# Optimization experiments

Hardware: AMD Instinct MI355X
Metric: run time of the kernel (lower is better)

Reference implementation:

```python
import jax, jax.numpy as jnp
import numpy as np

N_NODES = 100000
N_EDGES = 1600000
NFEAT, NHID, NCLASS = 256, 128, 40


def setup_inputs() -> dict:
    key = jax.random.key(0)
    ks = jax.random.split(key, 8)
    x = jax.random.normal(ks[0], (N_NODES, NFEAT), dtype=jnp.float32)
    edge_src = jax.random.randint(ks[1], (N_EDGES,), 0, N_NODES, dtype=jnp.int32)
    edge_dst = jax.random.randint(ks[2], (N_EDGES,), 0, N_NODES, dtype=jnp.int32)
    edge_weight = jax.random.uniform(ks[3], (N_EDGES,), dtype=jnp.float32)
    W1 = jax.random.normal(ks[4], (NFEAT, NHID), dtype=jnp.float32) * (1.0 / np.sqrt(NFEAT))
    b1 = jnp.zeros((NHID,), dtype=jnp.float32)
    W2 = jax.random.normal(ks[5], (NHID, NCLASS), dtype=jnp.float32) * (1.0 / np.sqrt(NHID))
    b2 = jnp.zeros((NCLASS,), dtype=jnp.float32)
    return {"x": x, "edge_src": edge_src, "edge_dst": edge_dst,
            "edge_weight": edge_weight, "W1": W1, "b1": b1, "W2": W2, "b2": b2}


def _spmm(edge_src, edge_dst, edge_weight, h):
    # out[i] = sum_{e: dst[e]==i} w[e] * h[src[e]]  (sparse adj @ h)
    msgs = edge_weight[:, None] * h[edge_src]            # [E, D]
    return jax.ops.segment_sum(msgs, edge_dst, num_segments=N_NODES)


def reference(x, edge_src, edge_dst, edge_weight, W1, b1, W2, b2):
    # GraphConvolution 1: adj @ (x @ W1) + b1, then ReLU
    h = _spmm(edge_src, edge_dst, edge_weight, x @ W1) + b1
    h = jax.nn.relu(h)
    # Dropout(p=0.5) is identity in eval/deterministic reference
    # GraphConvolution 2: adj @ (h @ W2) + b2
    out = _spmm(edge_src, edge_dst, edge_weight, h @ W2) + b2
    return out
```

## Files before the change

### kernel.cpp

```cpp
#include <hip/hip_runtime.h>

#define N_NODES 100000
#define N_EDGES 1600000
#define NFEAT 256
#define NHID 128
#define NCLASS 40

#define NGROUP 8
#define NODES_PER_GROUP 12500
#define NBKT 128
#define NPB 782
#define KPB (NPB * 8)
#define BCAP2 13200
#define EPB2 8192
#define NCH2 ((N_EDGES + EPB2 - 1) / EPB2)
#define NGEMM1 ((N_NODES + 127) / 128)
#define NKEY (N_NODES * 8)

using short8 = __attribute__((ext_vector_type(8))) short;
using f32x4 = __attribute__((ext_vector_type(4))) float;
using i32x4 = __attribute__((ext_vector_type(4))) int;
using i32x2 = __attribute__((ext_vector_type(2))) int;

__device__ inline float blo(unsigned u) { return __uint_as_float(u << 16); }
__device__ inline float bhi(unsigned u) { return __uint_as_float(u & 0xffff0000u); }
__device__ inline unsigned pk2(float a, float b) {
  unsigned x = __float_as_uint(a), y = __float_as_uint(b);
  unsigned lo = (x + 0x7FFFu + ((x >> 16) & 1u)) >> 16;
  unsigned hi = (y + 0x7FFFu + ((y >> 16) & 1u)) >> 16;
  return lo | (hi << 16);
}
__device__ inline unsigned short pk1(float a) {
  unsigned x = __float_as_uint(a);
  return (unsigned short)((x + 0x7FFFu + ((x >> 16) & 1u)) >> 16);
}


__global__ __launch_bounds__(512) void k_fatA(const int* __restrict__ src,
                                              const int* __restrict__ dst,
                                              const float* __restrict__ w,
                                              int* __restrict__ bcnt,
                                              int* __restrict__ bktK,
                                              i32x2* __restrict__ bktSW,
                                              const float* __restrict__ W1,
                                              unsigned short* __restrict__ w1s) {
  int tid = threadIdx.x;
  if (blockIdx.x >= NCH2) {
    int t = (blockIdx.x - NCH2) * 512 + tid;
    if (t < NFEAT * NHID) {
      int k = t >> 7, c = t & 127;
      int idx = (c * 256 + k) ^ ((c & 7) << 3);
      w1s[idx] = pk1(W1[t]);
    }
    return;
  }
  __shared__ int lcnt[NBKT], loff[NBKT], lcur[NBKT], lbase[NBKT];
  __shared__ int eK[EPB2];
  __shared__ i32x2 eSW[EPB2];
  if (tid < NBKT) lcnt[tid] = 0;
  __syncthreads();

  int base_e = blockIdx.x * EPB2;
  int nE = N_EDGES - base_e;
  if (nE > EPB2) nE = EPB2;
  int e0 = base_e + tid * 16;
  int key[16];
  i32x2 sw[16];
  bool full = (tid * 16 + 16 <= nE);
  if (full) {
#pragma unroll
    for (int g = 0; g < 4; g++) {
      i32x4 d4 = __builtin_nontemporal_load((const i32x4*)(dst + e0 + g * 4));
      i32x4 s4 = __builtin_nontemporal_load((const i32x4*)(src + e0 + g * 4));
      f32x4 w4 = __builtin_nontemporal_load((const f32x4*)(w + e0 + g * 4));
      int dd[4] = {d4.x, d4.y, d4.z, d4.w};
      int ss[4] = {s4.x, s4.y, s4.z, s4.w};
      float ww[4] = {w4.x, w4.y, w4.z, w4.w};
#pragma unroll
      for (int i = 0; i < 4; i++) {
        key[g * 4 + i] = dd[i] * 8 + (int)((unsigned)ss[i] / NODES_PER_GROUP);
        sw[g * 4 + i].x = ss[i];
        sw[g * 4 + i].y = __float_as_int(ww[i]);
        atomicAdd(&lcnt[(unsigned)dd[i] / NPB], 1);
      }
    }
  } else {
#pragma unroll
    for (int i = 0; i < 16; i++) {
      int e = tid * 16 + i;
      if (e < nE) {
        int d = dst[base_e + e], s = src[base_e + e];
        float ww = w[base_e + e];
        key[i] = d * 8 + (int)((unsigned)s / NODES_PER_GROUP);
        sw[i].x = s;
        sw[i].y = __float_as_int(ww);
        atomicAdd(&lcnt[(unsigned)d / NPB], 1);
      } else {
        key[i] = -1;
      }
    }
  }
  __syncthreads();
  if (tid < NBKT) loff[tid] = lcnt[tid];
  __syncthreads();
  for (int off = 1; off < NBKT; off <<= 1) {
    int u = (tid < NBKT && tid >= off) ? loff[tid - off] : 0;
    __syncthreads();
    if (tid < NBKT) loff[tid] += u;
    __syncthreads();
  }
  if (tid < NBKT) {
    int excl = loff[tid] - lcnt[tid];
    loff[tid] = excl;
    lcur[tid] = excl;
    lbase[tid] = atomicAdd(&bcnt[tid], lcnt[tid]);
  }
  __syncthreads();
#pragma unroll
  for (int i = 0; i < 16; i++) {
    if (key[i] >= 0) {
      int b = (unsigned)key[i] / KPB;
      int p = atomicAdd(&lcur[b], 1);
      eK[p] = key[i];
      eSW[p] = sw[i];
    }
  }
  __syncthreads();
  int wid = tid >> 6, lane = tid & 63;
  for (int b = wid; b < NBKT; b += 8) {
    int cnt = lcnt[b];
    int l0 = loff[b];
    int gb = lbase[b];
    if (gb + cnt > BCAP2) cnt = BCAP2 - gb;
    size_t g0 = (size_t)b * BCAP2 + gb;
    for (int i = lane; i < cnt; i += 64) {
      bktK[g0 + i] = eK[l0 + i];
      bktSW[g0 + i] = eSW[l0 + i];
    }
  }
}


__global__ __launch_bounds__(256) void k_gemm1(const float* __restrict__ x,
                                               const uint4* __restrict__ w1s,
                                               unsigned* __restrict__ h1u) {
  __shared__ char sB[65536];
  int tid = threadIdx.x;
  {
    uint4* dd = (uint4*)sB;
    for (int i = 0; i < 16; i++) dd[tid + i * 256] = w1s[tid + i * 256];
  }
  __syncthreads();

  int lane = tid & 63, wid = tid >> 6;
  int r16 = lane & 15, kgrp = lane >> 4;
  int rowbase = blockIdx.x * 128 + wid * 32;
  int ra0 = min(rowbase + r16, N_NODES - 1);
  int ra1 = min(rowbase + 16 + r16, N_NODES - 1);

  f32x4 acc[2][8];
#pragma unroll
  for (int m = 0; m < 2; m++)
#pragma unroll
    for (int n = 0; n < 8; n++) acc[m][n] = (f32x4){0.f, 0.f, 0.f, 0.f};

  for (int kt8 = 0; kt8 < 8; kt8++) {
    int k0 = kt8 * 32 + kgrp * 8;
    union { uint4 u; short8 s; } a[2];
#pragma unroll
    for (int m = 0; m < 2; m++) {
      const float* ap = x + (size_t)(m ? ra1 : ra0) * NFEAT + k0;
      float4 v0 = *(const float4*)ap;
      float4 v1 = *(const float4*)(ap + 4);
      a[m].u.x = pk2(v0.x, v0.y);
      a[m].u.y = pk2(v0.z, v0.w);
      a[m].u.z = pk2(v1.x, v1.y);
      a[m].u.w = pk2(v1.z, v1.w);
    }
#pragma unroll
    for (int n = 0; n < 8; n++) {
      int c = 16 * n + r16;
      int off = (c * 512 + k0 * 2) ^ ((c & 7) << 4);
      short8 b = *(const short8*)(sB + off);
      acc[0][n] = __builtin_amdgcn_mfma_f32_16x16x32_bf16(a[0].s, b, acc[0][n], 0, 0, 0);
      acc[1][n] = __builtin_amdgcn_mfma_f32_16x16x32_bf16(a[1].s, b, acc[1][n], 0, 0, 0);
    }
  }

#pragma unroll
  for (int m = 0; m < 2; m++) {
    int rb = rowbase + m * 16 + kgrp * 4;
#pragma unroll
    for (int n = 0; n < 8; n++) {
      f32x4 v = acc[m][n];
#pragma unroll
      for (int j = 0; j < 4; j++) {
        float o = __shfl_xor(v[j], 1);
        int row = rb + j;
        if (!(lane & 1) && row < N_NODES)
          h1u[(size_t)row * 64 + 8 * n + (r16 >> 1)] = pk2(v[j], o);
      }
    }
  }
}


__global__ void k_bbase(const int* __restrict__ bcnt, int* __restrict__ bbase) {
  __shared__ int s[NBKT];
  int t = threadIdx.x;
  int v = bcnt[t];
  s[t] = v;
  __syncthreads();
  for (int off = 1; off < NBKT; off <<= 1) {
    int u = (t >= off) ? s[t - off] : 0;
    __syncthreads();
    s[t] += u;
    __syncthreads();
  }
  bbase[t] = s[t] - v;
}


__global__ __launch_bounds__(1024) void k_build(const int* __restrict__ bcnt,
                                                const int* __restrict__ bbase,
                                                const int* __restrict__ bktK,
                                                const i32x2* __restrict__ bktSW,
                                                int* __restrict__ rp2,
                                                i32x2* __restrict__ esw) {
  __shared__ int lh[KPB];
  __shared__ int partial[1024];
  __shared__ i32x2 ebuf[BCAP2];

  int b = blockIdx.x;
  int t = threadIdx.x;
  int cnt = min(bcnt[b], BCAP2);
  int base = bbase[b];
  const int* kb = bktK + (size_t)b * BCAP2;
  const i32x2* sb = bktSW + (size_t)b * BCAP2;
  int k0 = b * KPB;

  for (int i = t; i < KPB; i += 1024) lh[i] = 0;
  __syncthreads();
  for (int i = t; i < cnt; i += 1024) atomicAdd(&lh[kb[i] - k0], 1);
  __syncthreads();

  int myoff = t * 7;
  int vals[7];
  int s0 = 0;
#pragma unroll
  for (int q = 0; q < 7; q++) {
    int i = myoff + q;
    int v = (i < KPB) ? lh[i] : 0;
    vals[q] = s0;
    s0 += v;
  }
  partial[t] = s0;
  __syncthreads();
  for (int off = 1; off < 1024; off <<= 1) {
    int u = (t >= off) ? partial[t - off] : 0;
    __syncthreads();
    partial[t] += u;
    __syncthreads();
  }
  int excl_base = partial[t] - s0;
  __syncthreads();
#pragma unroll
  for (int q = 0; q < 7; q++) {
    int i = myoff + q;
    if (i < KPB) {
      int e = excl_base + vals[q];
      int gk = k0 + i;
      if (gk < NKEY) rp2[gk] = base + e;
    }
  }
  __syncthreads();
#pragma unroll
  for (int q = 0; q < 7; q++) {
    int i = myoff + q;
    if (i < KPB) lh[i] = excl_base + vals[q];
  }
  if (b == NBKT - 1 && t == 0) rp2[NKEY] = N_EDGES;
  __syncthreads();

  for (int i = t; i < cnt; i += 1024) {
    int lk = kb[i] - k0;
    int pos = atomicAdd(&lh[lk], 1);
    ebuf[pos] = sb[i];
  }
  __syncthreads();

  i32x2* dstp = esw + base;
  for (int i = t; i < cnt; i += 1024) dstp[i] = ebuf[i];
}


__global__ __launch_bounds__(256) void k_spmm1(const unsigned* __restrict__ h1u,
                                               const int* __restrict__ rp2,
                                               const i32x2* __restrict__ esw,
                                               const float* __restrict__ bias1,
                                               unsigned* __restrict__ houtu) {
  int node = (blockIdx.x * 256 + threadIdx.x) >> 6;
  int lane = threadIdx.x & 63;
  if (node >= N_NODES) return;
  int beg = rp2[node * 8], end = rp2[node * 8 + 8];
  float aL0 = 0.f, aL1 = 0.f, aL2 = 0.f, aL3 = 0.f;
  float aH0 = 0.f, aH1 = 0.f, aH2 = 0.f, aH3 = 0.f;
  int j = beg;
  for (; j + 7 < end; j += 8) {
    i32x2 e0 = esw[j],     e1 = esw[j + 1], e2 = esw[j + 2], e3 = esw[j + 3];
    i32x2 e4 = esw[j + 4], e5 = esw[j + 5], e6 = esw[j + 6], e7 = esw[j + 7];
    unsigned u0 = h1u[((unsigned)e0.x << 6) + lane];
    unsigned u1 = h1u[((unsigned)e1.x << 6) + lane];
    unsigned u2 = h1u[((unsigned)e2.x << 6) + lane];
    unsigned u3 = h1u[((unsigned)e3.x << 6) + lane];
    unsigned u4 = h1u[((unsigned)e4.x << 6) + lane];
    unsigned u5 = h1u[((unsigned)e5.x << 6) + lane];
    unsigned u6 = h1u[((unsigned)e6.x << 6) + lane];
    unsigned u7 = h1u[((unsigned)e7.x << 6) + lane];
    float w0 = __int_as_float(e0.y), w1 = __int_as_float(e1.y);
    float w2 = __int_as_float(e2.y), w3 = __int_as_float(e3.y);
    float w4 = __int_as_float(e4.y), w5 = __int_as_float(e5.y);
    float w6 = __int_as_float(e6.y), w7 = __int_as_float(e7.y);
    aL0 = fmaf(w0, blo(u0), aL0); aH0 = fmaf(w0, bhi(u0), aH0);
    aL1 = fmaf(w1, blo(u1), aL1); aH1 = fmaf(w1, bhi(u1), aH1);
    aL2 = fmaf(w2, blo(u2), aL2); aH2 = fmaf(w2, bhi(u2), aH2);
    aL3 = fmaf(w3, blo(u3), aL3); aH3 = fmaf(w3, bhi(u3), aH3);
    aL0 = fmaf(w4, blo(u4), aL0); aH0 = fmaf(w4, bhi(u4), aH0);
    aL1 = fmaf(w5, blo(u5), aL1); aH1 = fmaf(w5, bhi(u5), aH1);
    aL2 = fmaf(w6, blo(u6), aL2); aH2 = fmaf(w6, bhi(u6), aH2);
    aL3 = fmaf(w7, blo(u7), aL3); aH3 = fmaf(w7, bhi(u7), aH3);
  }
  for (; j + 3 < end; j += 4) {
    i32x2 e0 = esw[j], e1 = esw[j + 1], e2 = esw[j + 2], e3 = esw[j + 3];
    unsigned u0 = h1u[((unsigned)e0.x << 6) + lane];
    unsigned u1 = h1u[((unsigned)e1.x << 6) + lane];
    unsigned u2 = h1u[((unsigned)e2.x << 6) + lane];
    unsigned u3 = h1u[((unsigned)e3.x << 6) + lane];
    float w0 = __int_as_float(e0.y), w1 = __int_as_float(e1.y);
    float w2 = __int_as_float(e2.y), w3 = __int_as_float(e3.y);
    aL0 = fmaf(w0, blo(u0), aL0); aH0 = fmaf(w0, bhi(u0), aH0);
    aL1 = fmaf(w1, blo(u1), aL1); aH1 = fmaf(w1, bhi(u1), aH1);
    aL2 = fmaf(w2, blo(u2), aL2); aH2 = fmaf(w2, bhi(u2), aH2);
    aL3 = fmaf(w3, blo(u3), aL3); aH3 = fmaf(w3, bhi(u3), aH3);
  }
  for (; j < end; j++) {
    i32x2 e0 = esw[j];
    unsigned u0 = h1u[((unsigned)e0.x << 6) + lane];
    float w0 = __int_as_float(e0.y);
    aL0 = fmaf(w0, blo(u0), aL0); aH0 = fmaf(w0, bhi(u0), aH0);
  }
  float r0 = (aL0 + aL1) + (aL2 + aL3) + bias1[2 * lane];
  float r1 = (aH0 + aH1) + (aH2 + aH3) + bias1[2 * lane + 1];
  houtu[(size_t)node * 64 + lane] = pk2(fmaxf(r0, 0.f), fmaxf(r1, 0.f));
}


__global__ __launch_bounds__(256) void k_gemm2(const unsigned* __restrict__ h_u,
                                               const float* __restrict__ W2,
                                               unsigned short* __restrict__ h2b) {
  __shared__ float hs[32][132];
  __shared__ float w2t[40][132];
  int tid = threadIdx.x;
  int row0 = blockIdx.x * 32;
  for (int i = tid; i < NHID * NCLASS; i += 256) {
    int k = i / NCLASS, c = i % NCLASS;
    w2t[c][k] = W2[i];
  }
  for (int i = tid; i < 2048; i += 256) {
    int r = i >> 6, c = i & 63;
    unsigned u = h_u[(size_t)(row0 + r) * 64 + c];
    hs[r][2 * c] = blo(u);
    hs[r][2 * c + 1] = bhi(u);
  }
  __syncthreads();
  int r = tid >> 3;
  int c0 = (tid & 7) * 5;
  float acc[5] = {0, 0, 0, 0, 0};
  for (int k = 0; k < NHID; k += 4) {
    float4 a = *(float4*)&hs[r][k];
#pragma unroll
    for (int j = 0; j < 5; j++) {
      float4 b = *(float4*)&w2t[c0 + j][k];
      acc[j] += a.x * b.x + a.y * b.y + a.z * b.z + a.w * b.w;
    }
  }
#pragma unroll
  for (int j = 0; j < 5; j++) h2b[(size_t)(row0 + r) * NCLASS + c0 + j] = pk1(acc[j]);
}


__global__ __launch_bounds__(256) void k_spmm2(const unsigned* __restrict__ h2u,
                                               const int* __restrict__ rp2,
                                               const i32x2* __restrict__ esw,
                                               const float* __restrict__ b2,
                                               float* __restrict__ out) {
  int node = (blockIdx.x * 256 + threadIdx.x) >> 6;
  int lane = threadIdx.x & 63;
  if (node >= N_NODES) return;
  int beg = rp2[node * 8], end = rp2[node * 8 + 8];
  int g = lane / 20;
  int jj = lane - g * 20;
  float aA0 = 0.f, aB0 = 0.f, aA1 = 0.f, aB1 = 0.f;
  if (g < 3) {
    int e = beg + g;
    for (; e + 3 < end; e += 6) {
      i32x2 p0 = esw[e];
      i32x2 p1 = esw[e + 3];
      unsigned u0 = h2u[(size_t)p0.x * 20 + jj];
      unsigned u1 = h2u[(size_t)p1.x * 20 + jj];
      float w0 = __int_as_float(p0.y), w1 = __int_as_float(p1.y);
      aA0 = fmaf(w0, blo(u0), aA0); aB0 = fmaf(w0, bhi(u0), aB0);
      aA1 = fmaf(w1, blo(u1), aA1); aB1 = fmaf(w1, bhi(u1), aB1);
    }
    if (e < end) {
      i32x2 p0 = esw[e];
      unsigned u0 = h2u[(size_t)p0.x * 20 + jj];
      float w0 = __int_as_float(p0.y);
      aA0 = fmaf(w0, blo(u0), aA0); aB0 = fmaf(w0, bhi(u0), aB0);
    }
  }
  float accA = aA0 + aA1, accB = aB0 + aB1;
  float tA = accA + __shfl(accA, lane + 20) + __shfl(accA, lane + 40);
  float tB = accB + __shfl(accB, lane + 20) + __shfl(accB, lane + 40);
  if (lane < 20) {
    float2 o = make_float2(tA + b2[2 * lane], tB + b2[2 * lane + 1]);
    *(float2*)&out[(size_t)node * NCLASS + 2 * lane] = o;
  }
}

extern "C" void kernel_launch(void* const* d_in, const int* in_sizes, int n_in,
                              void* d_out, int out_size, void* d_ws, size_t ws_size,
                              hipStream_t stream) {
  const float* x = (const float*)d_in[0];
  const int* src_in = (const int*)d_in[1];
  const int* dst_in = (const int*)d_in[2];
  const float* w_in = (const float*)d_in[3];
  const float* W1 = (const float*)d_in[4];
  const float* b1 = (const float*)d_in[5];
  const float* W2 = (const float*)d_in[6];
  const float* b2 = (const float*)d_in[7];
  float* out = (float*)d_out;

  unsigned short* h1b = (unsigned short*)d_ws;
  unsigned* hbuf = (unsigned*)(h1b + (size_t)N_NODES * NHID);
  unsigned short* h2b = (unsigned short*)(hbuf + (size_t)N_NODES * 64);
  i32x2* esw = (i32x2*)(h2b + (size_t)N_NODES * NCLASS);
  i32x2* bktSW = esw + N_EDGES;
  int* bktK = (int*)(bktSW + (size_t)NBKT * BCAP2);
  int* bcnt = bktK + (size_t)NBKT * BCAP2;
  int* bbase = bcnt + NBKT;
  int* rp2 = bbase + NBKT;
  unsigned short* w1s = (unsigned short*)(rp2 + NKEY + 4);

  hipMemsetAsync(bcnt, 0, NBKT * sizeof(int), stream);
  k_fatA<<<NCH2 + 64, 512, 0, stream>>>(src_in, dst_in, w_in, bcnt, bktK, bktSW, W1, w1s);
  k_gemm1<<<NGEMM1, 256, 0, stream>>>(x, (const uint4*)w1s, (unsigned*)h1b);
  k_bbase<<<1, NBKT, 0, stream>>>(bcnt, bbase);
  k_build<<<NBKT, 1024, 0, stream>>>(bcnt, bbase, bktK, bktSW, rp2, esw);

  k_spmm1<<<(N_NODES + 3) / 4, 256, 0, stream>>>((const unsigned*)h1b, rp2, esw, b1, hbuf);
  k_gemm2<<<N_NODES / 32, 256, 0, stream>>>(hbuf, W2, h2b);
  k_spmm2<<<(N_NODES + 3) / 4, 256, 0, stream>>>((const unsigned*)h2b, rp2, esw, b2, out);
}
```

Before: 227.8 us.

## Fold bucket scan into build, use nontemporal streams, vectorize edge loads

Removes the separate single-block prefix-scan launch by having every k_build block redundantly scan the 128 bucket counts in shared memory. Adds nontemporal load/store hints on streaming activation reads and writes in gemm1, spmm1, gemm2 and spmm2 so they are less likely to displace cached data. In spmm1, aligns the edge index to even and reads pairs of (src, weight) entries as 16-byte vectors instead of 8-byte loads. The trade-off is redundant scan work in each build block and the risk that nontemporal hints evict data that later kernels reuse.

```diff
diff --git a/kernel.cpp b/kernel.cpp
--- a/kernel.cpp
+++ b/kernel.cpp
@@ -19,6 +19,7 @@
 
 using short8 = __attribute__((ext_vector_type(8))) short;
 using f32x4 = __attribute__((ext_vector_type(4))) float;
+using f32x2 = __attribute__((ext_vector_type(2))) float;
 using i32x4 = __attribute__((ext_vector_type(4))) int;
 using i32x2 = __attribute__((ext_vector_type(2))) int;
 
@@ -170,8 +171,8 @@
 #pragma unroll
     for (int m = 0; m < 2; m++) {
       const float* ap = x + (size_t)(m ? ra1 : ra0) * NFEAT + k0;
-      float4 v0 = *(const float4*)ap;
-      float4 v1 = *(const float4*)(ap + 4);
+      f32x4 v0 = __builtin_nontemporal_load((const f32x4*)ap);
+      f32x4 v1 = __builtin_nontemporal_load((const f32x4*)(ap + 4));
       a[m].u.x = pk2(v0.x, v0.y);
       a[m].u.y = pk2(v0.z, v0.w);
       a[m].u.z = pk2(v1.x, v1.y);
@@ -198,43 +199,36 @@
         float o = __shfl_xor(v[j], 1);
         int row = rb + j;
         if (!(lane & 1) && row < N_NODES)
-          h1u[(size_t)row * 64 + 8 * n + (r16 >> 1)] = pk2(v[j], o);
+          __builtin_nontemporal_store(pk2(v[j], o),
+                                      &h1u[(size_t)row * 64 + 8 * n + (r16 >> 1)]);
       }
     }
   }
 }
 
 
-__global__ void k_bbase(const int* __restrict__ bcnt, int* __restrict__ bbase) {
-  __shared__ int s[NBKT];
-  int t = threadIdx.x;
-  int v = bcnt[t];
-  s[t] = v;
-  __syncthreads();
-  for (int off = 1; off < NBKT; off <<= 1) {
-    int u = (t >= off) ? s[t - off] : 0;
-    __syncthreads();
-    s[t] += u;
-    __syncthreads();
-  }
-  bbase[t] = s[t] - v;
-}
-
-
 __global__ __launch_bounds__(1024) void k_build(const int* __restrict__ bcnt,
-                                                const int* __restrict__ bbase,
                                                 const int* __restrict__ bktK,
                                                 const i32x2* __restrict__ bktSW,
                                                 int* __restrict__ rp2,
                                                 i32x2* __restrict__ esw) {
   __shared__ int lh[KPB];
   __shared__ int partial[1024];
+  __shared__ int sc[NBKT];
   __shared__ i32x2 ebuf[BCAP2];
 
   int b = blockIdx.x;
   int t = threadIdx.x;
+  if (t < NBKT) sc[t] = bcnt[t];
+  __syncthreads();
+  for (int off = 1; off < NBKT; off <<= 1) {
+    int u = (t < NBKT && t >= off) ? sc[t - off] : 0;
+    __syncthreads();
+    if (t < NBKT) sc[t] += u;
+    __syncthreads();
+  }
+  int base = (b == 0) ? 0 : sc[b - 1];
   int cnt = min(bcnt[b], BCAP2);
-  int base = bbase[b];
   const int* kb = bktK + (size_t)b * BCAP2;
   const i32x2* sb = bktSW + (size_t)b * BCAP2;
   int k0 = b * KPB;
@@ -306,21 +300,30 @@
   float aL0 = 0.f, aL1 = 0.f, aL2 = 0.f, aL3 = 0.f;
   float aH0 = 0.f, aH1 = 0.f, aH2 = 0.f, aH3 = 0.f;
   int j = beg;
+  if ((j & 1) && j < end) {
+    i32x2 e0 = esw[j];
+    unsigned u0 = h1u[((unsigned)e0.x << 6) + lane];
+    float w0 = __int_as_float(e0.y);
+    aL0 = fmaf(w0, blo(u0), aL0); aH0 = fmaf(w0, bhi(u0), aH0);
+    j++;
+  }
   for (; j + 7 < end; j += 8) {
-    i32x2 e0 = esw[j],     e1 = esw[j + 1], e2 = esw[j + 2], e3 = esw[j + 3];
-    i32x2 e4 = esw[j + 4], e5 = esw[j + 5], e6 = esw[j + 6], e7 = esw[j + 7];
-    unsigned u0 = h1u[((unsigned)e0.x << 6) + lane];
-    unsigned u1 = h1u[((unsigned)e1.x << 6) + lane];
-    unsigned u2 = h1u[((unsigned)e2.x << 6) + lane];
-    unsigned u3 = h1u[((unsigned)e3.x << 6) + lane];
-    unsigned u4 = h1u[((unsigned)e4.x << 6) + lane];
-    unsigned u5 = h1u[((unsigned)e5.x << 6) + lane];
-    unsigned u6 = h1u[((unsigned)e6.x << 6) + lane];
-    unsigned u7 = h1u[((unsigned)e7.x << 6) + lane];
-    float w0 = __int_as_float(e0.y), w1 = __int_as_float(e1.y);
-    float w2 = __int_as_float(e2.y), w3 = __int_as_float(e3.y);
-    float w4 = __int_as_float(e4.y), w5 = __int_as_float(e5.y);
-    float w6 = __int_as_float(e6.y), w7 = __int_as_float(e7.y);
+    i32x4 q0 = *(const i32x4*)(esw + j);
+    i32x4 q1 = *(const i32x4*)(esw + j + 2);
+    i32x4 q2 = *(const i32x4*)(esw + j + 4);
+    i32x4 q3 = *(const i32x4*)(esw + j + 6);
+    unsigned u0 = h1u[((unsigned)q0.x << 6) + lane];
+    unsigned u1 = h1u[((unsigned)q0.z << 6) + lane];
+    unsigned u2 = h1u[((unsigned)q1.x << 6) + lane];
+    unsigned u3 = h1u[((unsigned)q1.z << 6) + lane];
+    unsigned u4 = h1u[((unsigned)q2.x << 6) + lane];
+    unsigned u5 = h1u[((unsigned)q2.z << 6) + lane];
+    unsigned u6 = h1u[((unsigned)q3.x << 6) + lane];
+    unsigned u7 = h1u[((unsigned)q3.z << 6) + lane];
+    float w0 = __int_as_float(q0.y), w1 = __int_as_float(q0.w);
+    float w2 = __int_as_float(q1.y), w3 = __int_as_float(q1.w);
+    float w4 = __int_as_float(q2.y), w5 = __int_as_float(q2.w);
+    float w6 = __int_as_float(q3.y), w7 = __int_as_float(q3.w);
     aL0 = fmaf(w0, blo(u0), aL0); aH0 = fmaf(w0, bhi(u0), aH0);
     aL1 = fmaf(w1, blo(u1), aL1); aH1 = fmaf(w1, bhi(u1), aH1);
     aL2 = fmaf(w2, blo(u2), aL2); aH2 = fmaf(w2, bhi(u2), aH2);
@@ -330,20 +333,15 @@
     aL2 = fmaf(w6, blo(u6), aL2); aH2 = fmaf(w6, bhi(u6), aH2);
     aL3 = fmaf(w7, blo(u7), aL3); aH3 = fmaf(w7, bhi(u7), aH3);
   }
-  for (; j + 3 < end; j += 4) {
-    i32x2 e0 = esw[j], e1 = esw[j + 1], e2 = esw[j + 2], e3 = esw[j + 3];
-    unsigned u0 = h1u[((unsigned)e0.x << 6) + lane];
-    unsigned u1 = h1u[((unsigned)e1.x << 6) + lane];
-    unsigned u2 = h1u[((unsigned)e2.x << 6) + lane];
-    unsigned u3 = h1u[((unsigned)e3.x << 6) + lane];
-    float w0 = __int_as_float(e0.y), w1 = __int_as_float(e1.y);
-    float w2 = __int_as_float(e2.y), w3 = __int_as_float(e3.y);
+  for (; j + 1 < end; j += 2) {
+    i32x4 q0 = *(const i32x4*)(esw + j);
+    unsigned u0 = h1u[((unsigned)q0.x << 6) + lane];
+    unsigned u1 = h1u[((unsigned)q0.z << 6) + lane];
+    float w0 = __int_as_float(q0.y), w1 = __int_as_float(q0.w);
     aL0 = fmaf(w0, blo(u0), aL0); aH0 = fmaf(w0, bhi(u0), aH0);
     aL1 = fmaf(w1, blo(u1), aL1); aH1 = fmaf(w1, bhi(u1), aH1);
-    aL2 = fmaf(w2, blo(u2), aL2); aH2 = fmaf(w2, bhi(u2), aH2);
-    aL3 = fmaf(w3, blo(u3), aL3); aH3 = fmaf(w3, bhi(u3), aH3);
-  }
-  for (; j < end; j++) {
+  }
+  if (j < end) {
     i32x2 e0 = esw[j];
     unsigned u0 = h1u[((unsigned)e0.x << 6) + lane];
     float w0 = __int_as_float(e0.y);
@@ -351,7 +349,8 @@
   }
   float r0 = (aL0 + aL1) + (aL2 + aL3) + bias1[2 * lane];
   float r1 = (aH0 + aH1) + (aH2 + aH3) + bias1[2 * lane + 1];
-  houtu[(size_t)node * 64 + lane] = pk2(fmaxf(r0, 0.f), fmaxf(r1, 0.f));
+  __builtin_nontemporal_store(pk2(fmaxf(r0, 0.f), fmaxf(r1, 0.f)),
+                              &houtu[(size_t)node * 64 + lane]);
 }
 
 
@@ -368,7 +367,7 @@
   }
   for (int i = tid; i < 2048; i += 256) {
     int r = i >> 6, c = i & 63;
-    unsigned u = h_u[(size_t)(row0 + r) * 64 + c];
+    unsigned u = __builtin_nontemporal_load(h_u + (size_t)(row0 + r) * 64 + c);
     hs[r][2 * c] = blo(u);
     hs[r][2 * c + 1] = bhi(u);
   }
@@ -385,7 +384,8 @@
     }
   }
 #pragma unroll
-  for (int j = 0; j < 5; j++) h2b[(size_t)(row0 + r) * NCLASS + c0 + j] = pk1(acc[j]);
+  for (int j = 0; j < 5; j++)
+    __builtin_nontemporal_store(pk1(acc[j]), &h2b[(size_t)(row0 + r) * NCLASS + c0 + j]);
 }
 
 
@@ -423,8 +423,10 @@
   float tA = accA + __shfl(accA, lane + 20) + __shfl(accA, lane + 40);
   float tB = accB + __shfl(accB, lane + 20) + __shfl(accB, lane + 40);
   if (lane < 20) {
-    float2 o = make_float2(tA + b2[2 * lane], tB + b2[2 * lane + 1]);
-    *(float2*)&out[(size_t)node * NCLASS + 2 * lane] = o;
+    f32x2 o;
+    o.x = tA + b2[2 * lane];
+    o.y = tB + b2[2 * lane + 1];
+    __builtin_nontemporal_store(o, (f32x2*)&out[(size_t)node * NCLASS + 2 * lane]);
   }
 }
 
@@ -448,15 +450,13 @@
   i32x2* bktSW = esw + N_EDGES;
   int* bktK = (int*)(bktSW + (size_t)NBKT * BCAP2);
   int* bcnt = bktK + (size_t)NBKT * BCAP2;
-  int* bbase = bcnt + NBKT;
-  int* rp2 = bbase + NBKT;
+  int* rp2 = bcnt + NBKT;
   unsigned short* w1s = (unsigned short*)(rp2 + NKEY + 4);
 
   hipMemsetAsync(bcnt, 0, NBKT * sizeof(int), stream);
   k_fatA<<<NCH2 + 64, 512, 0, stream>>>(src_in, dst_in, w_in, bcnt, bktK, bktSW, W1, w1s);
   k_gemm1<<<NGEMM1, 256, 0, stream>>>(x, (const uint4*)w1s, (unsigned*)h1b);
-  k_bbase<<<1, NBKT, 0, stream>>>(bcnt, bbase);
-  k_build<<<NBKT, 1024, 0, stream>>>(bcnt, bbase, bktK, bktSW, rp2, esw);
+  k_build<<<NBKT, 1024, 0, stream>>>(bcnt, bktK, bktSW, rp2, esw);
 
   k_spmm1<<<(N_NODES + 3) / 4, 256, 0, stream>>>((const unsigned*)h1b, rp2, esw, b1, hbuf);
   k_gemm2<<<N_NODES / 32, 256, 0, stream>>>(hbuf, W2, h2b);
```

Result: slower. 244.6 us (+7.4%).
